# Optimization experiments

Measured on AMD Instinct MI355X. Metric: run time of the kernel, lower is better.

The kernel has to match this reference:

```python
import jax, jax.numpy as jnp
import numpy as np

M_HIST = 6
LAM = 1e-4
THRESHOLD = 50
BETA = 1.0


def _f_step(z, x, Wh, bh, Wx, bx, Wo, bo):
    # DEQ cell: f(z, x) = tanh(Linear(tanh(h_layer(x) + x_layer(z))))
    # (note: Func.forward(x, z) is called as f(z, x), so h_layer sees the
    #  external input x and x_layer sees the iterate z)
    hidden = jnp.tanh(x @ Wh.T + bh + z @ Wx.T + bx)  # [B,S,H]
    return jnp.tanh(hidden @ Wo.T + bo)               # [B,S,D]


def _anderson(f, x0):
    bsz = x0.shape[0]
    dL = x0.shape[1] * x0.shape[2]
    flat = lambda z: z.reshape(bsz, dL)
    unflat = lambda z: z.reshape(x0.shape)

    X = jnp.zeros((bsz, M_HIST, dL), dtype=x0.dtype)
    F = jnp.zeros((bsz, M_HIST, dL), dtype=x0.dtype)
    F0 = flat(f(x0))
    X = X.at[:, 0].set(flat(x0))
    F = F.at[:, 0].set(F0)
    X = X.at[:, 1].set(F0)
    F = F.at[:, 1].set(flat(f(unflat(F0))))

    lowest = jnp.asarray(1e8, dtype=x0.dtype)
    lowest_x = jnp.zeros((bsz, dL), dtype=x0.dtype)

    for k in range(2, THRESHOLD):  # fixed unrolled solver iterations
        n = min(k, M_HIST)
        G = F[:, :n] - X[:, :n]                       # [B,n,dL]
        GG = jnp.einsum('bnd,bmd->bnm', G, G) + LAM * jnp.eye(n, dtype=x0.dtype)
        H = jnp.zeros((bsz, n + 1, n + 1), dtype=x0.dtype)
        H = H.at[:, 0, 1:].set(1.0)
        H = H.at[:, 1:, 0].set(1.0)
        H = H.at[:, 1:, 1:].set(GG)
        rhs = jnp.zeros((bsz, n + 1, 1), dtype=x0.dtype).at[:, 0, 0].set(1.0)
        alpha = jnp.linalg.solve(H, rhs)[:, 1:, 0]    # [B,n]
        Xk = BETA * jnp.einsum('bn,bnd->bd', alpha, F[:, :n]) \
            + (1.0 - BETA) * jnp.einsum('bn,bnd->bd', alpha, X[:, :n])
        Fk = flat(f(unflat(Xk)))
        X = X.at[:, k % M_HIST].set(Xk)
        F = F.at[:, k % M_HIST].set(Fk)
        abs_diff = jnp.linalg.norm(Fk - Xk)
        rel_diff = abs_diff / (1e-5 + jnp.linalg.norm(Fk))
        better = rel_diff < lowest
        lowest_x = jnp.where(better, Xk, lowest_x)
        lowest = jnp.minimum(rel_diff, lowest)
    return unflat(lowest_x)


def setup_inputs() -> dict:
    key = jax.random.key(0)
    ks = jax.random.split(key, 9)
    B, S, D, H, O = 16384, 31, 14, 50, 1
    sc = lambda fan_in: 1.0 / np.sqrt(fan_in)
    return {
        'x':  jax.random.normal(ks[0], (B, S, D), jnp.float32),
        'Wh': jax.random.normal(ks[1], (H, D), jnp.float32) * sc(D),
        'bh': jax.random.normal(ks[2], (H,), jnp.float32) * sc(D),
        'Wx': jax.random.normal(ks[3], (H, D), jnp.float32) * sc(D),
        'bx': jax.random.normal(ks[4], (H,), jnp.float32) * sc(D),
        'Wo': jax.random.normal(ks[5], (D, H), jnp.float32) * sc(H),
        'bo': jax.random.normal(ks[6], (D,), jnp.float32) * sc(H),
        'Wf': jax.random.normal(ks[7], (O, S * D), jnp.float32) * sc(S * D),
        'bf': jax.random.normal(ks[8], (O,), jnp.float32) * sc(S * D),
    }


def reference(x, Wh, bh, Wx, bx, Wo, bo, Wf, bf):
    f = lambda z: _f_step(z, x, Wh, bh, Wx, bx, Wo, bo)
    z_star = _anderson(f, jnp.zeros_like(x))   # fixed-point solve (no grad)
    z = f(z_star)                              # one extra f application
    out = z.reshape(z.shape[0], -1) @ Wf.T + bf  # [B,1]
    return out
```

## Files before the change

### kernel.cpp

```cpp
#include <hip/hip_runtime.h>
#include <hip/hip_fp16.h>

#define S 31
#define D 14
#define H 50
#define NB 16384
#define NITER 48
#define LAMR 1e-4f

#define WS_D2   0
#define WS_F2   64
#define WS_WHP  128
#define WS_BHX  928
#define WS_BO   992
#define WS_WX2  1024
#define WS_WO2  1424
#define WS_WF2  1792
#define WS_OUTK 4096

typedef _Float16 f16x2 __attribute__((ext_vector_type(2)));

#if defined(__has_builtin) && __has_builtin(__builtin_amdgcn_rcpf)
#define FRCP(x) __builtin_amdgcn_rcpf(x)
#else
#define FRCP(x) (1.0f/(x))
#endif

#define FDOT2(a,b,c) __builtin_amdgcn_fdot2((a),(b),(c),false)

__device__ __forceinline__ f16x2 pkrtz(float a, float b){
  auto r = __builtin_amdgcn_cvt_pkrtz(a, b);
  return __builtin_bit_cast(f16x2, r);
}
#define PKRTZ(a,b) pkrtz((a),(b))

#define AIJ(i,j) ((i)*6 - ((i)*((i)+1))/2 + (j))

__device__ __forceinline__ float tfast(float x){
  float e = __expf(x + x);
  return 1.f - 2.f * FRCP(e + 1.f);
}

__device__ __forceinline__ float half_red(float v){
  v += __shfl_xor(v, 1);
  v += __shfl_xor(v, 2);
  v += __shfl_xor(v, 4);
  v += __shfl_xor(v, 8);
  v += __shfl_xor(v, 16);
  return v;
}

__global__ void prep_kernel(const float* __restrict__ Wh, const float* __restrict__ bh,
                            const float* __restrict__ Wx, const float* __restrict__ bx,
                            const float* __restrict__ Wo, const float* __restrict__ bo,
                            const float* __restrict__ Wf, float* __restrict__ ws){
  int t = threadIdx.x;
  for (int i=t;i<128;i+=256) ws[i]=0.f;
  for (int i=t;i<800;i+=256){
    int h=i>>4, d=i&15;
    ws[WS_WHP+i] = (d<D)? Wh[h*D+d] : 0.f;
  }
  for (int i=t;i<64;i+=256) ws[WS_BHX+i] = (i<H)? bh[i]+bx[i] : 0.f;
  for (int i=t;i<16;i+=256) ws[WS_BO+i]  = (i<D)? bo[i] : 0.f;
  __half2* wx2 = (__half2*)(ws + WS_WX2);
  for (int i=t;i<400;i+=256){
    int h=i>>3, dd=i&7, d0=2*dd, d1=2*dd+1;
    float a=(d0<D)?Wx[h*D+d0]:0.f, b=(d1<D)?Wx[h*D+d1]:0.f;
    wx2[i] = __floats2half2_rn(a,b);
  }
  __half2* wo2 = (__half2*)(ws + WS_WO2);
  for (int i=t;i<364;i+=256){
    int d=i/26, hh=i-26*d, h0=2*hh, h1=2*hh+1;
    float a=(hh<25)?Wo[d*H+h0]:0.f, b=(hh<25)?Wo[d*H+h1]:0.f;
    wo2[i] = __floats2half2_rn(a,b);
  }
  __half2* wf2 = (__half2*)(ws + WS_WF2);
  for (int i=t;i<256;i+=256){
    int s=i>>3, dd=i&7, d0=2*dd, d1=2*dd+1;
    float a=(s<S && d0<D)?Wf[s*D+d0]:0.f, b=(s<S && d1<D)?Wf[s*D+d1]:0.f;
    wf2[i] = __floats2half2_rn(a,b);
  }
}

#define FEVAL() do{ \
  f16x2 thh[25]; \
  _Pragma("unroll") \
  for (int hh_=0; hh_<25; ++hh_){ \
    float a0_ = hxr[2*hh_], b0_ = hxr[2*hh_+1]; \
    _Pragma("unroll") for (int q_=0;q_<7;++q_){ \
      a0_ = FDOT2(xvh[q_], wx2[(2*hh_)*8+q_],   a0_); \
      b0_ = FDOT2(xvh[q_], wx2[(2*hh_+1)*8+q_], b0_); } \
    thh[hh_] = PKRTZ(tfast(a0_), tfast(b0_)); \
  } \
  _Pragma("unroll") \
  for (int dp_=0; dp_<7; ++dp_){ \
    float t0_ = bop[2*dp_], t1_ = bop[2*dp_+1]; \
    float t0b_ = 0.f, t1b_ = 0.f; \
    _Pragma("unroll") for (int hh_=0;hh_<25;hh_+=2){ \
      t0_ = FDOT2(thh[hh_], wo2[(2*dp_)*26+hh_],   t0_); \
      t1_ = FDOT2(thh[hh_], wo2[(2*dp_+1)*26+hh_], t1_); } \
    _Pragma("unroll") for (int hh_=1;hh_<25;hh_+=2){ \
      t0b_ = FDOT2(thh[hh_], wo2[(2*dp_)*26+hh_],   t0b_); \
      t1b_ = FDOT2(thh[hh_], wo2[(2*dp_+1)*26+hh_], t1b_); } \
    fvh[dp_] = PKRTZ(tfast(t0_+t0b_), tfast(t1_+t1b_)); \
  } \
}while(0)

#define ZERO_INACT() do{ \
  if (!act){ \
    _Pragma("unroll") for (int q_=0;q_<7;++q_){ fvh[q_]=zzv; gvh[q_]=zzv; } \
  } \
}while(0)

#define PUSH() do{ \
  float dnew_[5]; \
  _Pragma("unroll") for (int j_=0;j_<5;++j_){ \
    float acc_=0.f; \
    _Pragma("unroll") for (int q_=0;q_<7;++q_) acc_ = FDOT2(gvh[q_], Gh[(j_+1)*7+q_], acc_); \
    dnew_[j_] = half_red(acc_); } \
  d2l=0.f; f2l=0.f; \
  _Pragma("unroll") for (int q_=0;q_<7;++q_){ \
    d2l = FDOT2(gvh[q_], gvh[q_], d2l); \
    f2l = FDOT2(fvh[q_], fvh[q_], f2l); } \
  d2r = half_red(d2l); f2r = half_red(f2l); \
  _Pragma("unroll") for (int j_=0;j_<5;++j_) \
    _Pragma("unroll") for (int q_=0;q_<7;++q_){ \
      Fh[j_*7+q_] = Fh[(j_+1)*7+q_]; Gh[j_*7+q_] = Gh[(j_+1)*7+q_]; } \
  _Pragma("unroll") for (int q_=0;q_<7;++q_){ Fh[35+q_]=fvh[q_]; Gh[35+q_]=gvh[q_]; } \
  _Pragma("unroll") for (int i_=0;i_<5;++i_) \
    _Pragma("unroll") for (int j_=i_;j_<5;++j_) GG[AIJ(i_,j_)] = GG[AIJ(i_+1,j_+1)]; \
  _Pragma("unroll") for (int j_=0;j_<5;++j_) GG[AIJ(j_,5)] = dnew_[j_]; \
  GG[AIJ(5,5)] = d2r; \
}while(0)

__global__ __launch_bounds__(256, 3)
void solver_kernel(const float* __restrict__ x,
                   const float* __restrict__ whp, const float* __restrict__ bhx,
                   const float* __restrict__ bop,
                   const f16x2* __restrict__ wx2, const f16x2* __restrict__ wo2,
                   const f16x2* __restrict__ wf2,
                   float* __restrict__ outk, float* __restrict__ d2p, float* __restrict__ f2p){
  const int tid  = threadIdx.x;
  const int lane = tid & 63;
  const int s    = tid & 31;
  const int elem = blockIdx.x*8 + (tid>>5);
  const bool act = (s < S);

  __shared__ float hx_sh[256*51];
  float* hxw = hx_sh + tid*51;

  {
    float xd[D];
#pragma unroll
    for (int d=0; d<D; ++d) xd[d]=0.f;
    if (act){
      const float* xr = x + ((size_t)elem*S + s)*D;
#pragma unroll
      for (int d=0; d<D; ++d) xd[d]=xr[d];
    }
#pragma unroll 2
    for (int h=0; h<H; ++h){
      float a0 = bhx[h], a1 = 0.f;
#pragma unroll
      for (int d=0; d<D; d+=2){ a0 += xd[d]*whp[h*16+d]; a1 += xd[d+1]*whp[h*16+d+1]; }
      hxw[h] = a0+a1;
    }
  }
  const float* hxr = hxw;
  const f16x2 zzv = {(_Float16)0.f, (_Float16)0.f};

  f16x2 Fh[42], Gh[42], xvh[7], fvh[7], gvh[7];
  float GG[21];
  float d2l, f2l, d2r, f2r;
#pragma unroll
  for (int i=0;i<42;++i){ Fh[i]=zzv; Gh[i]=zzv; }
#pragma unroll
  for (int i=0;i<21;++i) GG[i]=0.f;

#pragma unroll
  for (int q=0;q<7;++q) xvh[q]=zzv;
  FEVAL();
#pragma unroll
  for (int q=0;q<7;++q) gvh[q]=fvh[q]-xvh[q];
  ZERO_INACT();
  PUSH();
#pragma unroll
  for (int q=0;q<7;++q) xvh[q]=fvh[q];
  FEVAL();
#pragma unroll
  for (int q=0;q<7;++q) gvh[q]=fvh[q]-xvh[q];
  ZERO_INACT();
  PUSH();

#pragma unroll 1
  for (int kk=2; kk<50; ++kk){
    float A_[21], invd[6], yv[6];
    if (kk >= 6){
#pragma unroll
      for (int i=0;i<6;++i)
#pragma unroll
        for (int j=i;j<6;++j) A_[AIJ(i,j)] = GG[AIJ(i,j)] + ((i==j)?LAMR:0.f);
    } else {
      int lo = 6-kk;
#pragma unroll
      for (int i=0;i<6;++i)
#pragma unroll
        for (int j=i;j<6;++j){
          float v = GG[AIJ(i,j)] + ((i==j)?LAMR:0.f);
          A_[AIJ(i,j)] = (i>=lo)? v : ((i==j)?1e30f:0.f);
        }
    }
#pragma unroll
    for (int i=0;i<6;++i) yv[i]=1.f;
#pragma unroll
    for (int p=0;p<6;++p){
      invd[p] = FRCP(A_[AIJ(p,p)]);
#pragma unroll
      for (int i=p+1;i<6;++i){
        float m = A_[AIJ(p,i)]*invd[p];
#pragma unroll
        for (int j=i;j<6;++j) A_[AIJ(i,j)] -= m*A_[AIJ(p,j)];
        yv[i] -= m*yv[p];
      }
    }
#pragma unroll
    for (int p=5;p>=0;--p){
      float acc=yv[p];
#pragma unroll
      for (int j=p+1;j<6;++j) acc -= A_[AIJ(p,j)]*yv[j];
      yv[p]=acc*invd[p];
    }
    float isum = FRCP(yv[0]+yv[1]+yv[2]+yv[3]+yv[4]+yv[5]);
#pragma unroll
    for (int q=0;q<7;++q) xvh[q]=zzv;
#pragma unroll
    for (int j=0;j<6;++j){
      _Float16 ah = (_Float16)(yv[j]*isum);
      f16x2 a2 = {ah, ah};
#pragma unroll
      for (int q=0;q<7;++q) xvh[q] += a2*Fh[j*7+q];
    }
    FEVAL();
#pragma unroll
    for (int q=0;q<7;++q) gvh[q]=fvh[q]-xvh[q];
    ZERO_INACT();
    PUSH();
    float po=0.f;
    const f16x2* wfr = wf2 + s*8;
#pragma unroll
    for (int q=0;q<7;++q) po = FDOT2(fvh[q], wfr[q], po);
    po = half_red(po);
    float d2w = d2r + __shfl_xor(d2r, 32);
    float f2w = f2r + __shfl_xor(f2r, 32);
    if (lane==0){ atomicAdd(&d2p[kk-2], d2w); atomicAdd(&f2p[kk-2], f2w); }
    if (s==0) outk[(size_t)(kk-2)*NB + elem] = po;
  }
}

__global__ void final_kernel(const float* __restrict__ d2p, const float* __restrict__ f2p,
                             const float* __restrict__ outk, const float* __restrict__ bf,
                             float* __restrict__ out){
  int b = blockIdx.x*blockDim.x + threadIdx.x;
  float best = 1e8f; int kst = 0;
  for (int k=0;k<NITER;++k){
    float rel = sqrtf(d2p[k]) / (1e-5f + sqrtf(f2p[k]));
    if (rel < best){ best = rel; kst = k; }
  }
  out[b] = outk[(size_t)kst*NB + b] + bf[0];
}

extern "C" void kernel_launch(void* const* d_in, const int* in_sizes, int n_in,
                              void* d_out, int out_size, void* d_ws, size_t ws_size,
                              hipStream_t stream){
  const float* x  = (const float*)d_in[0];
  const float* Wh = (const float*)d_in[1];
  const float* bh = (const float*)d_in[2];
  const float* Wx = (const float*)d_in[3];
  const float* bx = (const float*)d_in[4];
  const float* Wo = (const float*)d_in[5];
  const float* bo = (const float*)d_in[6];
  const float* Wf = (const float*)d_in[7];
  const float* bf = (const float*)d_in[8];
  float* ws  = (float*)d_ws;
  float* out = (float*)d_out;

  hipLaunchKernelGGL(prep_kernel, dim3(1), dim3(256), 0, stream, Wh,bh,Wx,bx,Wo,bo,Wf,ws);
  hipLaunchKernelGGL(solver_kernel, dim3(NB/8), dim3(256), 0, stream,
                     x, ws+WS_WHP, ws+WS_BHX, ws+WS_BO,
                     (const f16x2*)(ws+WS_WX2), (const f16x2*)(ws+WS_WO2), (const f16x2*)(ws+WS_WF2),
                     ws+WS_OUTK, ws+WS_D2, ws+WS_F2);
  hipLaunchKernelGGL(final_kernel, dim3(NB/256), dim3(256), 0, stream,
                     ws+WS_D2, ws+WS_F2, ws+WS_OUTK, bf, out);
}
```

Baseline: 3.275 ms.

## Prescale weights for exp2 tanh, stage weights and fp16 hx in LDS, cut registers

Folds the 2*log2(e) factor into the weights and biases on the host-side prep so tanh uses exp2 directly without a multiply. The per-thread hidden-input cache moves from fp32 with a 51-float stride to packed fp16 pairs in an interleaved LDS layout. The Wx, Wo, Wf and bo tables are also copied into LDS. The gvh register array is dropped by reusing xvh, and the invd array by storing reciprocals in place, to lower register pressure. The risks are fp16 rounding of the precomputed hx and the extra LDS traffic and synchronisation.

```diff
diff --git a/kernel.cpp b/kernel.cpp
--- a/kernel.cpp
+++ b/kernel.cpp
@@ -7,6 +7,7 @@
 #define NB 16384
 #define NITER 48
 #define LAMR 1e-4f
+#define SC 2.8853900817779268f
 
 #define WS_D2   0
 #define WS_F2   64
@@ -15,7 +16,7 @@
 #define WS_BO   992
 #define WS_WX2  1024
 #define WS_WO2  1424
-#define WS_WF2  1792
+#define WS_WF2  1824
 #define WS_OUTK 4096
 
 typedef _Float16 f16x2 __attribute__((ext_vector_type(2)));
@@ -34,12 +35,12 @@
 }
 #define PKRTZ(a,b) pkrtz((a),(b))
 
+__device__ __forceinline__ float tsc(float u){
+  float e = __builtin_exp2f(u);
+  return 1.f - 2.f * FRCP(e + 1.f);
+}
+
 #define AIJ(i,j) ((i)*6 - ((i)*((i)+1))/2 + (j))
-
-__device__ __forceinline__ float tfast(float x){
-  float e = __expf(x + x);
-  return 1.f - 2.f * FRCP(e + 1.f);
-}
 
 __device__ __forceinline__ float half_red(float v){
   v += __shfl_xor(v, 1);
@@ -58,20 +59,20 @@
   for (int i=t;i<128;i+=256) ws[i]=0.f;
   for (int i=t;i<800;i+=256){
     int h=i>>4, d=i&15;
-    ws[WS_WHP+i] = (d<D)? Wh[h*D+d] : 0.f;
-  }
-  for (int i=t;i<64;i+=256) ws[WS_BHX+i] = (i<H)? bh[i]+bx[i] : 0.f;
-  for (int i=t;i<16;i+=256) ws[WS_BO+i]  = (i<D)? bo[i] : 0.f;
+    ws[WS_WHP+i] = (d<D)? Wh[h*D+d]*SC : 0.f;
+  }
+  for (int i=t;i<64;i+=256) ws[WS_BHX+i] = (i<H)? (bh[i]+bx[i])*SC : 0.f;
+  for (int i=t;i<16;i+=256) ws[WS_BO+i]  = (i<D)? bo[i]*SC : 0.f;
   __half2* wx2 = (__half2*)(ws + WS_WX2);
   for (int i=t;i<400;i+=256){
     int h=i>>3, dd=i&7, d0=2*dd, d1=2*dd+1;
-    float a=(d0<D)?Wx[h*D+d0]:0.f, b=(d1<D)?Wx[h*D+d1]:0.f;
+    float a=(d0<D)?Wx[h*D+d0]*SC:0.f, b=(d1<D)?Wx[h*D+d1]*SC:0.f;
     wx2[i] = __floats2half2_rn(a,b);
   }
   __half2* wo2 = (__half2*)(ws + WS_WO2);
-  for (int i=t;i<364;i+=256){
-    int d=i/26, hh=i-26*d, h0=2*hh, h1=2*hh+1;
-    float a=(hh<25)?Wo[d*H+h0]:0.f, b=(hh<25)?Wo[d*H+h1]:0.f;
+  for (int i=t;i<392;i+=256){
+    int d=i/28, hh=i-28*d;
+    float a=(hh<25)?Wo[d*H+2*hh]*SC:0.f, b=(hh<25)?Wo[d*H+2*hh+1]*SC:0.f;
     wo2[i] = __floats2half2_rn(a,b);
   }
   __half2* wf2 = (__half2*)(ws + WS_WF2);
@@ -86,29 +87,30 @@
   f16x2 thh[25]; \
   _Pragma("unroll") \
   for (int hh_=0; hh_<25; ++hh_){ \
-    float a0_ = hxr[2*hh_], b0_ = hxr[2*hh_+1]; \
+    f16x2 hx2_ = hxs[hh_*256 + tid]; \
+    float a0_ = (float)hx2_.x, b0_ = (float)hx2_.y; \
     _Pragma("unroll") for (int q_=0;q_<7;++q_){ \
-      a0_ = FDOT2(xvh[q_], wx2[(2*hh_)*8+q_],   a0_); \
-      b0_ = FDOT2(xvh[q_], wx2[(2*hh_+1)*8+q_], b0_); } \
-    thh[hh_] = PKRTZ(tfast(a0_), tfast(b0_)); \
+      a0_ = FDOT2(xvh[q_], wxs[(2*hh_)*8+q_],   a0_); \
+      b0_ = FDOT2(xvh[q_], wxs[(2*hh_+1)*8+q_], b0_); } \
+    thh[hh_] = PKRTZ(tsc(a0_), tsc(b0_)); \
   } \
   _Pragma("unroll") \
   for (int dp_=0; dp_<7; ++dp_){ \
-    float t0_ = bop[2*dp_], t1_ = bop[2*dp_+1]; \
+    float t0_ = bos[2*dp_], t1_ = bos[2*dp_+1]; \
     float t0b_ = 0.f, t1b_ = 0.f; \
     _Pragma("unroll") for (int hh_=0;hh_<25;hh_+=2){ \
-      t0_ = FDOT2(thh[hh_], wo2[(2*dp_)*26+hh_],   t0_); \
-      t1_ = FDOT2(thh[hh_], wo2[(2*dp_+1)*26+hh_], t1_); } \
+      t0_ = FDOT2(thh[hh_], wos[(2*dp_)*28+hh_],   t0_); \
+      t1_ = FDOT2(thh[hh_], wos[(2*dp_+1)*28+hh_], t1_); } \
     _Pragma("unroll") for (int hh_=1;hh_<25;hh_+=2){ \
-      t0b_ = FDOT2(thh[hh_], wo2[(2*dp_)*26+hh_],   t0b_); \
-      t1b_ = FDOT2(thh[hh_], wo2[(2*dp_+1)*26+hh_], t1b_); } \
-    fvh[dp_] = PKRTZ(tfast(t0_+t0b_), tfast(t1_+t1b_)); \
+      t0b_ = FDOT2(thh[hh_], wos[(2*dp_)*28+hh_],   t0b_); \
+      t1b_ = FDOT2(thh[hh_], wos[(2*dp_+1)*28+hh_], t1b_); } \
+    fvh[dp_] = PKRTZ(tsc(t0_+t0b_), tsc(t1_+t1b_)); \
   } \
 }while(0)
 
 #define ZERO_INACT() do{ \
   if (!act){ \
-    _Pragma("unroll") for (int q_=0;q_<7;++q_){ fvh[q_]=zzv; gvh[q_]=zzv; } \
+    _Pragma("unroll") for (int q_=0;q_<7;++q_){ fvh[q_]=zzv; xvh[q_]=zzv; } \
   } \
 }while(0)
 
@@ -116,17 +118,17 @@
   float dnew_[5]; \
   _Pragma("unroll") for (int j_=0;j_<5;++j_){ \
     float acc_=0.f; \
-    _Pragma("unroll") for (int q_=0;q_<7;++q_) acc_ = FDOT2(gvh[q_], Gh[(j_+1)*7+q_], acc_); \
+    _Pragma("unroll") for (int q_=0;q_<7;++q_) acc_ = FDOT2(xvh[q_], Gh[(j_+1)*7+q_], acc_); \
     dnew_[j_] = half_red(acc_); } \
-  d2l=0.f; f2l=0.f; \
+  float d2l=0.f, f2l=0.f; \
   _Pragma("unroll") for (int q_=0;q_<7;++q_){ \
-    d2l = FDOT2(gvh[q_], gvh[q_], d2l); \
+    d2l = FDOT2(xvh[q_], xvh[q_], d2l); \
     f2l = FDOT2(fvh[q_], fvh[q_], f2l); } \
   d2r = half_red(d2l); f2r = half_red(f2l); \
   _Pragma("unroll") for (int j_=0;j_<5;++j_) \
     _Pragma("unroll") for (int q_=0;q_<7;++q_){ \
       Fh[j_*7+q_] = Fh[(j_+1)*7+q_]; Gh[j_*7+q_] = Gh[(j_+1)*7+q_]; } \
-  _Pragma("unroll") for (int q_=0;q_<7;++q_){ Fh[35+q_]=fvh[q_]; Gh[35+q_]=gvh[q_]; } \
+  _Pragma("unroll") for (int q_=0;q_<7;++q_){ Fh[35+q_]=fvh[q_]; Gh[35+q_]=xvh[q_]; } \
   _Pragma("unroll") for (int i_=0;i_<5;++i_) \
     _Pragma("unroll") for (int j_=i_;j_<5;++j_) GG[AIJ(i_,j_)] = GG[AIJ(i_+1,j_+1)]; \
   _Pragma("unroll") for (int j_=0;j_<5;++j_) GG[AIJ(j_,5)] = dnew_[j_]; \
@@ -136,9 +138,9 @@
 __global__ __launch_bounds__(256, 3)
 void solver_kernel(const float* __restrict__ x,
                    const float* __restrict__ whp, const float* __restrict__ bhx,
-                   const float* __restrict__ bop,
-                   const f16x2* __restrict__ wx2, const f16x2* __restrict__ wo2,
-                   const f16x2* __restrict__ wf2,
+                   const float* __restrict__ bopg,
+                   const f16x2* __restrict__ wx2g, const f16x2* __restrict__ wo2g,
+                   const f16x2* __restrict__ wf2g,
                    float* __restrict__ outk, float* __restrict__ d2p, float* __restrict__ f2p){
   const int tid  = threadIdx.x;
   const int lane = tid & 63;
@@ -146,8 +148,16 @@
   const int elem = blockIdx.x*8 + (tid>>5);
   const bool act = (s < S);
 
-  __shared__ float hx_sh[256*51];
-  float* hxw = hx_sh + tid*51;
+  __shared__ f16x2 hxs[25*256];
+  __shared__ f16x2 wxs[400];
+  __shared__ f16x2 wos[392];
+  __shared__ f16x2 wfs[256];
+  __shared__ float bos[16];
+
+  for (int i=tid;i<400;i+=256) wxs[i]=wx2g[i];
+  for (int i=tid;i<392;i+=256) wos[i]=wo2g[i];
+  if (tid<256) wfs[tid]=wf2g[tid];
+  if (tid<16)  bos[tid]=bopg[tid];
 
   {
     float xd[D];
@@ -158,20 +168,24 @@
 #pragma unroll
       for (int d=0; d<D; ++d) xd[d]=xr[d];
     }
-#pragma unroll 2
-    for (int h=0; h<H; ++h){
-      float a0 = bhx[h], a1 = 0.f;
-#pragma unroll
-      for (int d=0; d<D; d+=2){ a0 += xd[d]*whp[h*16+d]; a1 += xd[d+1]*whp[h*16+d+1]; }
-      hxw[h] = a0+a1;
-    }
-  }
-  const float* hxr = hxw;
+#pragma unroll 1
+    for (int hh=0; hh<25; ++hh){
+      float a0 = bhx[2*hh], a1 = 0.f, b0 = bhx[2*hh+1], b1 = 0.f;
+#pragma unroll
+      for (int d=0; d<D; d+=2){
+        a0 += xd[d]*whp[(2*hh)*16+d];   a1 += xd[d+1]*whp[(2*hh)*16+d+1];
+        b0 += xd[d]*whp[(2*hh+1)*16+d]; b1 += xd[d+1]*whp[(2*hh+1)*16+d+1];
+      }
+      hxs[hh*256+tid] = PKRTZ(a0+a1, b0+b1);
+    }
+  }
+  __syncthreads();
+
   const f16x2 zzv = {(_Float16)0.f, (_Float16)0.f};
 
-  f16x2 Fh[42], Gh[42], xvh[7], fvh[7], gvh[7];
+  f16x2 Fh[42], Gh[42], xvh[7], fvh[7];
   float GG[21];
-  float d2l, f2l, d2r, f2r;
+  float d2r, f2r;
 #pragma unroll
   for (int i=0;i<42;++i){ Fh[i]=zzv; Gh[i]=zzv; }
 #pragma unroll
@@ -181,20 +195,20 @@
   for (int q=0;q<7;++q) xvh[q]=zzv;
   FEVAL();
 #pragma unroll
-  for (int q=0;q<7;++q) gvh[q]=fvh[q]-xvh[q];
+  for (int q=0;q<7;++q) xvh[q]=fvh[q]-xvh[q];
   ZERO_INACT();
   PUSH();
 #pragma unroll
-  for (int q=0;q<7;++q) xvh[q]=fvh[q];
+  for (int q=0;q<7;++q) xvh[q]=Fh[35+q];
   FEVAL();
 #pragma unroll
-  for (int q=0;q<7;++q) gvh[q]=fvh[q]-xvh[q];
+  for (int q=0;q<7;++q) xvh[q]=fvh[q]-xvh[q];
   ZERO_INACT();
   PUSH();
 
 #pragma unroll 1
   for (int kk=2; kk<50; ++kk){
-    float A_[21], invd[6], yv[6];
+    float A_[21], yv[6];
     if (kk >= 6){
 #pragma unroll
       for (int i=0;i<6;++i)
@@ -214,10 +228,11 @@
     for (int i=0;i<6;++i) yv[i]=1.f;
 #pragma unroll
     for (int p=0;p<6;++p){
-      invd[p] = FRCP(A_[AIJ(p,p)]);
+      float inv = FRCP(A_[AIJ(p,p)]);
+      A_[AIJ(p,p)] = inv;
 #pragma unroll
       for (int i=p+1;i<6;++i){
-        float m = A_[AIJ(p,i)]*invd[p];
+        float m = A_[AIJ(p,i)]*inv;
 #pragma unroll
         for (int j=i;j<6;++j) A_[AIJ(i,j)] -= m*A_[AIJ(p,j)];
         yv[i] -= m*yv[p];
@@ -228,7 +243,7 @@
       float acc=yv[p];
 #pragma unroll
       for (int j=p+1;j<6;++j) acc -= A_[AIJ(p,j)]*yv[j];
-      yv[p]=acc*invd[p];
+      yv[p]=acc*A_[AIJ(p,p)];
     }
     float isum = FRCP(yv[0]+yv[1]+yv[2]+yv[3]+yv[4]+yv[5]);
 #pragma unroll
@@ -242,11 +257,11 @@
     }
     FEVAL();
 #pragma unroll
-    for (int q=0;q<7;++q) gvh[q]=fvh[q]-xvh[q];
+    for (int q=0;q<7;++q) xvh[q]=fvh[q]-xvh[q];
     ZERO_INACT();
     PUSH();
     float po=0.f;
-    const f16x2* wfr = wf2 + s*8;
+    const f16x2* wfr = wfs + s*8;
 #pragma unroll
     for (int q=0;q<7;++q) po = FDOT2(fvh[q], wfr[q], po);
     po = half_red(po);
```

Measured after the change: 6.062 ms. +85.1%, slower.
